# Kernel tuning notes

Hardware: AMD Instinct MI355X
Metric: run time of the kernel (lower is better)

## Reference

```python
import jax, jax.numpy as jnp
import numpy as np

B, D, T = 8, 256, 2048


def setup_inputs() -> dict:
    key = jax.random.key(0)
    k1, k2, k3, k4 = jax.random.split(key, 4)
    return {
        "inputs_r": jax.random.normal(k1, (B, D, T), dtype=jnp.float32),
        "inputs_i": jax.random.normal(k2, (B, D, T), dtype=jnp.float32),
        "filters_r": jax.random.normal(k3, (B, D, T), dtype=jnp.float32),
        "filters_i": jax.random.normal(k4, (B, D, T), dtype=jnp.float32),
        "L": 2,
        "I": 1,
    }


def reference(inputs_r, inputs_i, filters_r, filters_i, L, I):
    # Torch uses a one-hot eye conv2d kernel to unfold (2I+1)x(2L+1) windows
    # over (freq D, time T) with zero padding (I, L), then does a channel-wise
    # complex-ish multiply and sums over the window channels. Faithful fused
    # form: accumulate shifted products over the small fixed window, never
    # materializing the [2B, (2I+1)(2L+1), D, T] unfolds.
    tw, fw = 2 * L + 1, 2 * I + 1
    Bn, Dn, Tn = inputs_r.shape
    pad = lambda a: jnp.pad(a, ((0, 0), (I, I), (L, L)))
    xr_p, xi_p = pad(inputs_r), pad(inputs_i)
    fr_p, fi_p = pad(filters_r), pad(filters_i)
    out_r = jnp.zeros_like(inputs_r)
    out_i = jnp.zeros_like(inputs_r)
    for kf in range(fw):          # freq taps (small, fixed)
        for kt in range(tw):      # time taps (small, fixed)
            sl = lambda a: a[:, kf:kf + Dn, kt:kt + Tn]
            r, im = sl(xr_p), sl(xi_p)
            fr, fi = sl(fr_p), sl(fi_p)
            out_r = out_r + r * fr - im * fi
            # NOTE: faithful to the source bug: inputs_r*filters_i appears twice
            out_i = out_i + 2.0 * r * fi
    return jnp.concatenate([out_r, out_i], axis=1)  # [B, 2D, T]
```

## Files before the change

kernel.cpp:

```cpp
#include <hip/hip_runtime.h>


#define BB 8
#define DD 256
#define TT_FULL 2048
#define DTILE 8
#define TTILE 128
#define RROWS (DTILE + 2)
#define RCOLS4 34
#define LSTRIDE 136

__global__ __launch_bounds__(256) void deepfilter_kernel(
    const float* __restrict__ xr, const float* __restrict__ xi,
    const float* __restrict__ fr, const float* __restrict__ fi,
    float* __restrict__ out)
{
    __shared__ float Pr[RROWS][LSTRIDE];
    __shared__ float Pi[RROWS][LSTRIDE];

    const int tt  = blockIdx.x;
    const int dt  = blockIdx.y;
    const int b   = blockIdx.z;
    const int t0  = tt * TTILE;
    const int d0  = dt * DTILE;
    const int tid = threadIdx.x;

    const size_t base_in = (size_t)b * DD * TT_FULL;

    #pragma unroll
    for (int k = 0; k < 2; ++k) {
        const int idx = tid + k * 256;
        if (idx < RROWS * RCOLS4) {
            const int row = idx / RCOLS4;
            const int c4  = idx - row * RCOLS4;
            const int d   = d0 + row - 1;
            const int tg  = t0 - 4 + (c4 << 2);
            float4 pr4 = {0.f, 0.f, 0.f, 0.f};
            float4 pi4 = {0.f, 0.f, 0.f, 0.f};
            if ((unsigned)d < (unsigned)DD) {
                const size_t roff = base_in + (size_t)d * TT_FULL;
                float4 r4, i4, g4, h4;
                if (tg >= 0 && tg <= TT_FULL - 4) {
                    r4 = *(const float4*)(xr + roff + tg);
                    i4 = *(const float4*)(xi + roff + tg);
                    g4 = *(const float4*)(fr + roff + tg);
                    h4 = *(const float4*)(fi + roff + tg);
                } else {
                    float rr[4], ii[4], gg[4], hh[4];
                    #pragma unroll
                    for (int j = 0; j < 4; ++j) {
                        const int t = tg + j;
                        const bool ok = (unsigned)t < (unsigned)TT_FULL;
                        rr[j] = ok ? xr[roff + t] : 0.f;
                        ii[j] = ok ? xi[roff + t] : 0.f;
                        gg[j] = ok ? fr[roff + t] : 0.f;
                        hh[j] = ok ? fi[roff + t] : 0.f;
                    }
                    r4 = make_float4(rr[0], rr[1], rr[2], rr[3]);
                    i4 = make_float4(ii[0], ii[1], ii[2], ii[3]);
                    g4 = make_float4(gg[0], gg[1], gg[2], gg[3]);
                    h4 = make_float4(hh[0], hh[1], hh[2], hh[3]);
                }
                pr4.x = r4.x * g4.x - i4.x * h4.x;
                pr4.y = r4.y * g4.y - i4.y * h4.y;
                pr4.z = r4.z * g4.z - i4.z * h4.z;
                pr4.w = r4.w * g4.w - i4.w * h4.w;
                pi4.x = 2.f * r4.x * h4.x;
                pi4.y = 2.f * r4.y * h4.y;
                pi4.z = 2.f * r4.z * h4.z;
                pi4.w = 2.f * r4.w * h4.w;
            }
            *(float4*)&Pr[row][c4 << 2] = pr4;
            *(float4*)&Pi[row][c4 << 2] = pi4;
        }
    }
    __syncthreads();

    const int orow = tid >> 5;
    const int oc   = (tid & 31) << 2;

    float4 Ar = {0,0,0,0}, Br = {0,0,0,0};
    float2 Cr = {0,0};
    float4 Ai = {0,0,0,0}, Bi = {0,0,0,0};
    float2 Ci = {0,0};
    #pragma unroll
    for (int kf = 0; kf < 3; ++kf) {
        const float* rp = &Pr[orow + kf][oc];
        const float* ip = &Pi[orow + kf][oc];
        float4 v0 = *(const float4*)rp;
        float4 v1 = *(const float4*)(rp + 4);
        float2 v2 = *(const float2*)(rp + 8);
        Ar.x += v0.x; Ar.y += v0.y; Ar.z += v0.z; Ar.w += v0.w;
        Br.x += v1.x; Br.y += v1.y; Br.z += v1.z; Br.w += v1.w;
        Cr.x += v2.x; Cr.y += v2.y;
        float4 w0 = *(const float4*)ip;
        float4 w1 = *(const float4*)(ip + 4);
        float2 w2 = *(const float2*)(ip + 8);
        Ai.x += w0.x; Ai.y += w0.y; Ai.z += w0.z; Ai.w += w0.w;
        Bi.x += w1.x; Bi.y += w1.y; Bi.z += w1.z; Bi.w += w1.w;
        Ci.x += w2.x; Ci.y += w2.y;
    }

    float4 outr, outi;
    {
        const float s0 = Ar.z, s1 = Ar.w, s2 = Br.x, s3 = Br.y,
                    s4 = Br.z, s5 = Br.w, s6 = Cr.x, s7 = Cr.y;
        const float m = s3 + s4;
        const float a = s1 + s2 + m;
        const float bmid = s2 + m + s5;
        outr.x = s0 + a;
        outr.y = a + s5;
        outr.z = bmid + s6;
        outr.w = m + s5 + s6 + s7;
    }
    {
        const float s0 = Ai.z, s1 = Ai.w, s2 = Bi.x, s3 = Bi.y,
                    s4 = Bi.z, s5 = Bi.w, s6 = Ci.x, s7 = Ci.y;
        const float m = s3 + s4;
        const float a = s1 + s2 + m;
        const float bmid = s2 + m + s5;
        outi.x = s0 + a;
        outi.y = a + s5;
        outi.z = bmid + s6;
        outi.w = m + s5 + s6 + s7;
    }

    const size_t obase = (size_t)b * (2 * DD * TT_FULL)
                       + (size_t)(d0 + orow) * TT_FULL + (t0 + oc);
    *(float4*)&out[obase] = outr;
    *(float4*)&out[obase + (size_t)DD * TT_FULL] = outi;
}

extern "C" void kernel_launch(void* const* d_in, const int* in_sizes, int n_in,
                              void* d_out, int out_size, void* d_ws, size_t ws_size,
                              hipStream_t stream) {
    const float* xr = (const float*)d_in[0];
    const float* xi = (const float*)d_in[1];
    const float* fr = (const float*)d_in[2];
    const float* fi = (const float*)d_in[3];
    float* out = (float*)d_out;

    dim3 grid(TT_FULL / TTILE, DD / DTILE, BB);
    deepfilter_kernel<<<grid, 256, 0, stream>>>(xr, xi, fr, fi, out);
}
```

Measured before the change: 113.1 us.

## Process four time chunks per block with double-buffered register prefetch

Each block now loops over four consecutive 128-wide time chunks. The next chunk's global loads are issued into registers before the current chunk is reduced from LDS, and the products go into a second LDS buffer. This aims to hide global load latency and amortise block setup over more work. In exchange the grid has a quarter as many blocks, and per-thread register use and LDS size both rise. The halo columns are still reloaded for every chunk.

```diff
diff --git a/kernel.cpp b/kernel.cpp
--- a/kernel.cpp
+++ b/kernel.cpp
@@ -6,40 +6,53 @@
 #define TT_FULL 2048
 #define DTILE 8
 #define TTILE 128
+#define CHUNKS 4
 #define RROWS (DTILE + 2)
 #define RCOLS4 34
 #define LSTRIDE 136
+#define NSLOTS (RROWS * RCOLS4)
 
-__global__ __launch_bounds__(256) void deepfilter_kernel(
+__global__ __launch_bounds__(256, 4) void deepfilter_kernel(
     const float* __restrict__ xr, const float* __restrict__ xi,
     const float* __restrict__ fr, const float* __restrict__ fi,
     float* __restrict__ out)
 {
-    __shared__ float Pr[RROWS][LSTRIDE];
-    __shared__ float Pi[RROWS][LSTRIDE];
+    __shared__ float Pr[2][RROWS][LSTRIDE];
+    __shared__ float Pi[2][RROWS][LSTRIDE];
 
-    const int tt  = blockIdx.x;
+    const int tg0 = blockIdx.x * (TTILE * CHUNKS);
     const int dt  = blockIdx.y;
     const int b   = blockIdx.z;
-    const int t0  = tt * TTILE;
     const int d0  = dt * DTILE;
     const int tid = threadIdx.x;
 
     const size_t base_in = (size_t)b * DD * TT_FULL;
 
+    const int nslot = (tid < NSLOTS - 256) ? 2 : 1;
+    int srow[2], sc4[2];
+    bool sok[2];
+    size_t sroff[2];
     #pragma unroll
-    for (int k = 0; k < 2; ++k) {
-        const int idx = tid + k * 256;
-        if (idx < RROWS * RCOLS4) {
-            const int row = idx / RCOLS4;
-            const int c4  = idx - row * RCOLS4;
-            const int d   = d0 + row - 1;
-            const int tg  = t0 - 4 + (c4 << 2);
-            float4 pr4 = {0.f, 0.f, 0.f, 0.f};
-            float4 pi4 = {0.f, 0.f, 0.f, 0.f};
-            if ((unsigned)d < (unsigned)DD) {
-                const size_t roff = base_in + (size_t)d * TT_FULL;
-                float4 r4, i4, g4, h4;
+    for (int s = 0; s < 2; ++s) {
+        const int idx = tid + s * 256;
+        srow[s] = idx / RCOLS4;
+        sc4[s]  = idx - srow[s] * RCOLS4;
+        const int d = d0 + srow[s] - 1;
+        sok[s] = ((unsigned)d < (unsigned)DD) && (idx < NSLOTS);
+        sroff[s] = base_in + (size_t)d * TT_FULL;
+    }
+
+    float4 sR[2], sI[2], sG[2], sH[2];
+
+    auto LOAD = [&](int t0) {
+        #pragma unroll
+        for (int s = 0; s < 2; ++s) {
+            if (s && nslot < 2) break;
+            float4 r4 = {0,0,0,0}, i4 = {0,0,0,0};
+            float4 g4 = {0,0,0,0}, h4 = {0,0,0,0};
+            if (sok[s]) {
+                const int tg = t0 - 4 + (sc4[s] << 2);
+                const size_t roff = sroff[s];
                 if (tg >= 0 && tg <= TT_FULL - 4) {
                     r4 = *(const float4*)(xr + roff + tg);
                     i4 = *(const float4*)(xi + roff + tg);
@@ -50,85 +63,110 @@
                     #pragma unroll
                     for (int j = 0; j < 4; ++j) {
                         const int t = tg + j;
-                        const bool ok = (unsigned)t < (unsigned)TT_FULL;
-                        rr[j] = ok ? xr[roff + t] : 0.f;
-                        ii[j] = ok ? xi[roff + t] : 0.f;
-                        gg[j] = ok ? fr[roff + t] : 0.f;
-                        hh[j] = ok ? fi[roff + t] : 0.f;
+                        const bool okt = (unsigned)t < (unsigned)TT_FULL;
+                        rr[j] = okt ? xr[roff + t] : 0.f;
+                        ii[j] = okt ? xi[roff + t] : 0.f;
+                        gg[j] = okt ? fr[roff + t] : 0.f;
+                        hh[j] = okt ? fi[roff + t] : 0.f;
                     }
                     r4 = make_float4(rr[0], rr[1], rr[2], rr[3]);
                     i4 = make_float4(ii[0], ii[1], ii[2], ii[3]);
                     g4 = make_float4(gg[0], gg[1], gg[2], gg[3]);
                     h4 = make_float4(hh[0], hh[1], hh[2], hh[3]);
                 }
-                pr4.x = r4.x * g4.x - i4.x * h4.x;
-                pr4.y = r4.y * g4.y - i4.y * h4.y;
-                pr4.z = r4.z * g4.z - i4.z * h4.z;
-                pr4.w = r4.w * g4.w - i4.w * h4.w;
-                pi4.x = 2.f * r4.x * h4.x;
-                pi4.y = 2.f * r4.y * h4.y;
-                pi4.z = 2.f * r4.z * h4.z;
-                pi4.w = 2.f * r4.w * h4.w;
             }
-            *(float4*)&Pr[row][c4 << 2] = pr4;
-            *(float4*)&Pi[row][c4 << 2] = pi4;
+            sR[s] = r4; sI[s] = i4; sG[s] = g4; sH[s] = h4;
         }
-    }
-    __syncthreads();
+    };
+
+    auto STORE_LDS = [&](int buf) {
+        #pragma unroll
+        for (int s = 0; s < 2; ++s) {
+            if (s && nslot < 2) break;
+            const float4 r4 = sR[s], i4 = sI[s], g4 = sG[s], h4 = sH[s];
+            float4 pr4, pi4;
+            pr4.x = r4.x * g4.x - i4.x * h4.x;
+            pr4.y = r4.y * g4.y - i4.y * h4.y;
+            pr4.z = r4.z * g4.z - i4.z * h4.z;
+            pr4.w = r4.w * g4.w - i4.w * h4.w;
+            pi4.x = 2.f * r4.x * h4.x;
+            pi4.y = 2.f * r4.y * h4.y;
+            pi4.z = 2.f * r4.z * h4.z;
+            pi4.w = 2.f * r4.w * h4.w;
+            *(float4*)&Pr[buf][srow[s]][sc4[s] << 2] = pr4;
+            *(float4*)&Pi[buf][srow[s]][sc4[s] << 2] = pi4;
+        }
+    };
 
     const int orow = tid >> 5;
     const int oc   = (tid & 31) << 2;
 
-    float4 Ar = {0,0,0,0}, Br = {0,0,0,0};
-    float2 Cr = {0,0};
-    float4 Ai = {0,0,0,0}, Bi = {0,0,0,0};
-    float2 Ci = {0,0};
+    auto COMPUTE = [&](int buf, int t0) {
+        float4 Ar = {0,0,0,0}, Br = {0,0,0,0};
+        float2 Cr = {0,0};
+        float4 Ai = {0,0,0,0}, Bi = {0,0,0,0};
+        float2 Ci = {0,0};
+        #pragma unroll
+        for (int kf = 0; kf < 3; ++kf) {
+            const float* rp = &Pr[buf][orow + kf][oc];
+            const float* ip = &Pi[buf][orow + kf][oc];
+            float4 v0 = *(const float4*)rp;
+            float4 v1 = *(const float4*)(rp + 4);
+            float2 v2 = *(const float2*)(rp + 8);
+            Ar.x += v0.x; Ar.y += v0.y; Ar.z += v0.z; Ar.w += v0.w;
+            Br.x += v1.x; Br.y += v1.y; Br.z += v1.z; Br.w += v1.w;
+            Cr.x += v2.x; Cr.y += v2.y;
+            float4 w0 = *(const float4*)ip;
+            float4 w1 = *(const float4*)(ip + 4);
+            float2 w2 = *(const float2*)(ip + 8);
+            Ai.x += w0.x; Ai.y += w0.y; Ai.z += w0.z; Ai.w += w0.w;
+            Bi.x += w1.x; Bi.y += w1.y; Bi.z += w1.z; Bi.w += w1.w;
+            Ci.x += w2.x; Ci.y += w2.y;
+        }
+
+        float4 outr, outi;
+        {
+            const float s0 = Ar.z, s1 = Ar.w, s2 = Br.x, s3 = Br.y,
+                        s4 = Br.z, s5 = Br.w, s6 = Cr.x, s7 = Cr.y;
+            const float m = s3 + s4;
+            const float a = s1 + s2 + m;
+            const float bmid = s2 + m + s5;
+            outr.x = s0 + a;
+            outr.y = a + s5;
+            outr.z = bmid + s6;
+            outr.w = m + s5 + s6 + s7;
+        }
+        {
+            const float s0 = Ai.z, s1 = Ai.w, s2 = Bi.x, s3 = Bi.y,
+                        s4 = Bi.z, s5 = Bi.w, s6 = Ci.x, s7 = Ci.y;
+            const float m = s3 + s4;
+            const float a = s1 + s2 + m;
+            const float bmid = s2 + m + s5;
+            outi.x = s0 + a;
+            outi.y = a + s5;
+            outi.z = bmid + s6;
+            outi.w = m + s5 + s6 + s7;
+        }
+
+        const size_t obase = (size_t)b * (2 * DD * TT_FULL)
+                           + (size_t)(d0 + orow) * TT_FULL + (t0 + oc);
+        *(float4*)&out[obase] = outr;
+        *(float4*)&out[obase + (size_t)DD * TT_FULL] = outi;
+    };
+
+    LOAD(tg0);
+    STORE_LDS(0);
+    __syncthreads();
+
     #pragma unroll
-    for (int kf = 0; kf < 3; ++kf) {
-        const float* rp = &Pr[orow + kf][oc];
-        const float* ip = &Pi[orow + kf][oc];
-        float4 v0 = *(const float4*)rp;
-        float4 v1 = *(const float4*)(rp + 4);
-        float2 v2 = *(const float2*)(rp + 8);
-        Ar.x += v0.x; Ar.y += v0.y; Ar.z += v0.z; Ar.w += v0.w;
-        Br.x += v1.x; Br.y += v1.y; Br.z += v1.z; Br.w += v1.w;
-        Cr.x += v2.x; Cr.y += v2.y;
-        float4 w0 = *(const float4*)ip;
-        float4 w1 = *(const float4*)(ip + 4);
-        float2 w2 = *(const float2*)(ip + 8);
-        Ai.x += w0.x; Ai.y += w0.y; Ai.z += w0.z; Ai.w += w0.w;
-        Bi.x += w1.x; Bi.y += w1.y; Bi.z += w1.z; Bi.w += w1.w;
-        Ci.x += w2.x; Ci.y += w2.y;
+    for (int k = 0; k < CHUNKS; ++k) {
+        if (k + 1 < CHUNKS) LOAD(tg0 + (k + 1) * TTILE);
+        COMPUTE(k & 1, tg0 + k * TTILE);
+        if (k + 1 < CHUNKS) {
+            STORE_LDS((k + 1) & 1);
+            __syncthreads();
+        }
     }
-
-    float4 outr, outi;
-    {
-        const float s0 = Ar.z, s1 = Ar.w, s2 = Br.x, s3 = Br.y,
-                    s4 = Br.z, s5 = Br.w, s6 = Cr.x, s7 = Cr.y;
-        const float m = s3 + s4;
-        const float a = s1 + s2 + m;
-        const float bmid = s2 + m + s5;
-        outr.x = s0 + a;
-        outr.y = a + s5;
-        outr.z = bmid + s6;
-        outr.w = m + s5 + s6 + s7;
-    }
-    {
-        const float s0 = Ai.z, s1 = Ai.w, s2 = Bi.x, s3 = Bi.y,
-                    s4 = Bi.z, s5 = Bi.w, s6 = Ci.x, s7 = Ci.y;
-        const float m = s3 + s4;
-        const float a = s1 + s2 + m;
-        const float bmid = s2 + m + s5;
-        outi.x = s0 + a;
-        outi.y = a + s5;
-        outi.z = bmid + s6;
-        outi.w = m + s5 + s6 + s7;
-    }
-
-    const size_t obase = (size_t)b * (2 * DD * TT_FULL)
-                       + (size_t)(d0 + orow) * TT_FULL + (t0 + oc);
-    *(float4*)&out[obase] = outr;
-    *(float4*)&out[obase + (size_t)DD * TT_FULL] = outi;
 }
 
 extern "C" void kernel_launch(void* const* d_in, const int* in_sizes, int n_in,
@@ -140,6 +178,6 @@
     const float* fi = (const float*)d_in[3];
     float* out = (float*)d_out;
 
-    dim3 grid(TT_FULL / TTILE, DD / DTILE, BB);
+    dim3 grid(TT_FULL / (TTILE * CHUNKS), DD / DTILE, BB);
     deepfilter_kernel<<<grid, 256, 0, stream>>>(xr, xi, fr, fi, out);
 }
```

After: 114.0 us. No clear change (+0.8%).
